# Kernel optimization log

Hardware: AMD Instinct MI355X
Metric: run time of the kernel (lower is better)

## Reference

```python
import jax, jax.numpy as jnp
import numpy as np

N_NODES = 100000
N_EDGES = 3200000
IN_F = 256
OUT_F = 256


def setup_inputs() -> dict:
    key = jax.random.key(0)
    k1, k2, k3, k4, k5, k6 = jax.random.split(key, 6)
    x = jax.random.normal(k1, (N_NODES, IN_F), dtype=jnp.float32)
    edge_row = jnp.sort(jax.random.randint(k2, (N_EDGES,), 0, N_NODES, dtype=jnp.int64))
    edge_col = jax.random.randint(k3, (N_EDGES,), 0, N_NODES, dtype=jnp.int64)
    edge_val = jax.random.uniform(k4, (N_EDGES,), dtype=jnp.float32)
    stdv = 1.0 / np.sqrt(OUT_F)
    weight = jax.random.uniform(k5, (IN_F, OUT_F), dtype=jnp.float32, minval=-stdv, maxval=stdv)
    bias = jax.random.uniform(k6, (OUT_F,), dtype=jnp.float32, minval=-stdv, maxval=stdv)
    return {"x": x, "edge_row": edge_row, "edge_col": edge_col,
            "edge_val": edge_val, "weight": weight, "bias": bias}


def reference(x, edge_row, edge_col, edge_val, weight, bias):
    # support = x @ W  -> [N, out]
    support = jnp.matmul(x, weight)
    # spmm(adj, support): out[r] = sum_e val[e] * support[col[e]] for edges with row[e]==r
    gathered = support[edge_col] * edge_val[:, None]  # [E, out]
    output = jax.ops.segment_sum(gathered, edge_row, num_segments=N_NODES)
    return output + bias
```

## Files before the change

kernel.cpp:

```cpp
#include <hip/hip_runtime.h>
#include <hip/hip_bf16.h>

#define NN 100000
#define NE 3200000
#define NF 256
#define CHUNK 512

typedef __attribute__((ext_vector_type(8))) __bf16 bf16x8;
typedef __attribute__((ext_vector_type(4))) float  f32x4;


__global__ __launch_bounds__(256) void prep_all(const float* __restrict__ w,
                                                __bf16* __restrict__ wfrag,
                                                const float* __restrict__ bias,
                                                float* __restrict__ bias_p,
                                                const int* __restrict__ erow,
                                                int* __restrict__ rowptr) {
    if (blockIdx.x >= 33) {
        const int e = (blockIdx.x - 33) * 256 + threadIdx.x;
        if (e >= NE) return;
        const int r    = erow[e];
        const int prev = (e == 0) ? -1 : erow[e - 1];
        for (int q = prev + 1; q <= r; ++q) rowptr[q] = e;
        if (e == NE - 1) {
            for (int q = r + 1; q <= NN; ++q) rowptr[q] = NE;
        }
        return;
    }
    if (blockIdx.x == 32) {
        const int t = threadIdx.x;
        const int l = t >> 2, b = t & 3;
        bias_p[t] = bias[(l & 3) * 64 + 16 * b + (l >> 2)];
        return;
    }
    const int t = blockIdx.x * 256 + threadIdx.x;
    const int lane = t & 63;
    const int nf   = (t >> 6) & 15;
    const int ks   = t >> 10;
    const int col  = nf * 16 + (lane & 15);
    const int k0   = ks * 32 + (lane >> 4) * 8;
    bf16x8 v;
#pragma unroll
    for (int j = 0; j < 8; ++j) v[j] = (__bf16)w[(k0 + j) * NF + col];
    reinterpret_cast<bf16x8*>(wfrag)[t] = v;
}

__global__ __launch_bounds__(320) void gemm_q(const float* __restrict__ x,
                                              const __bf16* __restrict__ wfrag,
                                              unsigned char* __restrict__ tab,
                                              float* __restrict__ scales) {
    __shared__ __align__(16) __bf16 As[80 * 72];

    const int t    = threadIdx.x;
    const int wv   = t >> 6;
    const int lane = t & 63;
    const int row0 = blockIdx.x * 80;

    f32x4 acc[16];
#pragma unroll
    for (int nf = 0; nf < 16; ++nf) acc[nf] = (f32x4){0.f, 0.f, 0.f, 0.f};

    const int    srow = t >> 2;
    const int    sc   = (t & 3) * 16;
    const float* xp   = x + (size_t)(row0 + srow) * NF + sc;
    char* const  wr   = reinterpret_cast<char*>(As) + srow * 144 + sc * 2;

    const char* const rd =
        reinterpret_cast<const char*>(As) + (wv * 16 + (lane & 15)) * 144 + ((lane >> 4) << 4);

    const bf16x8* wf = reinterpret_cast<const bf16x8*>(wfrag);

    f32x4 s0 = __builtin_nontemporal_load(reinterpret_cast<const f32x4*>(xp));
    f32x4 s1 = __builtin_nontemporal_load(reinterpret_cast<const f32x4*>(xp + 4));
    f32x4 s2 = __builtin_nontemporal_load(reinterpret_cast<const f32x4*>(xp + 8));
    f32x4 s3 = __builtin_nontemporal_load(reinterpret_cast<const f32x4*>(xp + 12));

    for (int p = 0; p < 4; ++p) {
        bf16x8 b0, b1;
        b0[0] = (__bf16)s0.x; b0[1] = (__bf16)s0.y; b0[2] = (__bf16)s0.z; b0[3] = (__bf16)s0.w;
        b0[4] = (__bf16)s1.x; b0[5] = (__bf16)s1.y; b0[6] = (__bf16)s1.z; b0[7] = (__bf16)s1.w;
        b1[0] = (__bf16)s2.x; b1[1] = (__bf16)s2.y; b1[2] = (__bf16)s2.z; b1[3] = (__bf16)s2.w;
        b1[4] = (__bf16)s3.x; b1[5] = (__bf16)s3.y; b1[6] = (__bf16)s3.z; b1[7] = (__bf16)s3.w;
        *reinterpret_cast<bf16x8*>(wr)      = b0;
        *reinterpret_cast<bf16x8*>(wr + 16) = b1;
        __syncthreads();

        if (p < 3) {
            const float* nx = xp + (p + 1) * 64;
            s0 = __builtin_nontemporal_load(reinterpret_cast<const f32x4*>(nx));
            s1 = __builtin_nontemporal_load(reinterpret_cast<const f32x4*>(nx + 4));
            s2 = __builtin_nontemporal_load(reinterpret_cast<const f32x4*>(nx + 8));
            s3 = __builtin_nontemporal_load(reinterpret_cast<const f32x4*>(nx + 12));
        }

        const bf16x8 af0 = *reinterpret_cast<const bf16x8*>(rd);
        const bf16x8 af1 = *reinterpret_cast<const bf16x8*>(rd + 64);
#pragma unroll
        for (int nf = 0; nf < 16; ++nf) {
            const bf16x8 w0 = wf[((p * 2 + 0) * 16 + nf) * 64 + lane];
            acc[nf] = __builtin_amdgcn_mfma_f32_16x16x32_bf16(af0, w0, acc[nf], 0, 0, 0);
        }
#pragma unroll
        for (int nf = 0; nf < 16; ++nf) {
            const bf16x8 w1 = wf[((p * 2 + 1) * 16 + nf) * 64 + lane];
            acc[nf] = __builtin_amdgcn_mfma_f32_16x16x32_bf16(af1, w1, acc[nf], 0, 0, 0);
        }
        __syncthreads();
    }

    const int hi   = lane >> 4;
    const int ccol = lane & 15;

    float m[4];
#pragma unroll
    for (int r = 0; r < 4; ++r) {
        float mm = 0.f;
#pragma unroll
        for (int nf = 0; nf < 16; ++nf) mm = fmaxf(mm, fabsf(acc[nf][r]));
        m[r] = mm;
    }
#pragma unroll
    for (int w = 1; w < 16; w <<= 1) {
#pragma unroll
        for (int r = 0; r < 4; ++r) m[r] = fmaxf(m[r], __shfl_xor(m[r], w, 64));
    }

#pragma unroll
    for (int r = 0; r < 4; ++r) {
        const int   node = row0 + wv * 16 + hi * 4 + r;
        const float isc  = 127.0f / fmaxf(m[r], 1e-30f);
        uint4 pk = {0u, 0u, 0u, 0u};
        unsigned int* pw = reinterpret_cast<unsigned int*>(&pk);
#pragma unroll
        for (int nf = 0; nf < 16; ++nf) {
            const int q = (int)rintf(acc[nf][r] * isc) + 128;
            pw[nf >> 2] |= ((unsigned int)(q & 0xff)) << ((nf & 3) * 8);
        }
        *reinterpret_cast<uint4*>(tab + (size_t)node * 256 + ccol * 16) = pk;
        if (ccol == 0) scales[node] = m[r] * (1.0f / 127.0f);
    }
}

__global__ __launch_bounds__(256) void spmm_f(const unsigned int* __restrict__ tab32,
                                              const int* __restrict__ rowptr,
                                              const int* __restrict__ ecol,
                                              const float* __restrict__ eval,
                                              const float* __restrict__ scales,
                                              const float* __restrict__ bias_p,
                                              float* __restrict__ out) {
    __shared__ int2 buf[CHUNK];

    const int wave = threadIdx.x >> 6;
    const int lane = threadIdx.x & 63;
    const int row  = blockIdx.x * 4 + wave;

    const int bs   = rowptr[blockIdx.x * 4];
    const int bend = rowptr[blockIdx.x * 4 + 4];
    const int rs   = rowptr[row];
    const int re   = rowptr[row + 1];

    float a0 = 0.f, a1 = 0.f, a2 = 0.f, a3 = 0.f, S = 0.f;

    for (int cs = bs; cs < bend; cs += CHUNK) {
        const int cnt = min(CHUNK, bend - cs);
        if (cs != bs) __syncthreads();
        for (int j = threadIdx.x; j < cnt; j += 256) {
            const int   c = ecol[cs + j];
            const float v = eval[cs + j];
            buf[j] = make_int2(c, __float_as_int(v * scales[c]));
        }
        __syncthreads();

        const int lo = max(rs, cs);
        const int hi = min(re, cs + cnt);
#pragma unroll 4
        for (int i = lo; i < hi; ++i) {
            const int2  p = buf[i - cs];
            const float v = __int_as_float(p.y);
            const unsigned int g = tab32[((unsigned)p.x << 6) + lane];
            a0 = fmaf(v, (float)(g & 0xffu), a0);
            a1 = fmaf(v, (float)((g >> 8) & 0xffu), a1);
            a2 = fmaf(v, (float)((g >> 16) & 0xffu), a2);
            a3 = fmaf(v, (float)(g >> 24), a3);
            S += v;
        }
    }

    const f32x4 bp = *reinterpret_cast<const f32x4*>(bias_p + lane * 4);
    const float c128 = 128.0f * S;
    float* op = out + (size_t)row * NF + (lane & 3) * 64 + (lane >> 2);
    __builtin_nontemporal_store(a0 - c128 + bp.x, op);
    __builtin_nontemporal_store(a1 - c128 + bp.y, op + 16);
    __builtin_nontemporal_store(a2 - c128 + bp.z, op + 32);
    __builtin_nontemporal_store(a3 - c128 + bp.w, op + 48);
}

extern "C" void kernel_launch(void* const* d_in, const int* in_sizes, int n_in,
                              void* d_out, int out_size, void* d_ws, size_t ws_size,
                              hipStream_t stream) {
    const float* x    = (const float*)d_in[0];
    const int*   erow = (const int*)d_in[1];
    const int*   ecol = (const int*)d_in[2];
    const float* eval = (const float*)d_in[3];
    const float* w    = (const float*)d_in[4];
    const float* bias = (const float*)d_in[5];
    float*       out  = (float*)d_out;

    unsigned char* tab    = (unsigned char*)d_ws;
    int*           rowptr = (int*)((char*)d_ws + 25600000);
    __bf16*        wfrag  = (__bf16*)((char*)d_ws + 26000016);
    float*         scales = (float*)((char*)d_ws + 26131088);
    float*         bias_p = (float*)((char*)d_ws + 26531088);

    prep_all<<<33 + (NE + 255) / 256, 256, 0, stream>>>(w, wfrag, bias, bias_p,
                                                        erow, rowptr);
    gemm_q<<<NN / 80, 320, 0, stream>>>(x, wfrag, tab, scales);
    spmm_f<<<NN / 4, 256, 0, stream>>>(
        reinterpret_cast<const unsigned int*>(tab), rowptr, ecol, eval, scales,
        bias_p, out);
}
```

Measured before the change: 196.5 us.

## Reuse weight fragments across two row tiles per wave and vectorize rowptr build

The GEMM kernel now uses 128-row blocks of 4 waves, each wave computing two 16-row tiles. Every weight fragment loaded from global memory therefore feeds two MFMAs, halving weight traffic per output row, with bounds clamping for the partial last block. The rowptr construction now has each thread handle 8 sorted edges using vectorized loads, cutting thread count and redundant neighbor reads. Doubling the accumulators raises register pressure, which the launch bounds of 2 blocks per SM try to contain.

Result: slower. 214.2 us (+9.0%).

```diff
diff --git a/kernel.cpp b/kernel.cpp
--- a/kernel.cpp
+++ b/kernel.cpp
@@ -8,6 +8,7 @@
 
 typedef __attribute__((ext_vector_type(8))) __bf16 bf16x8;
 typedef __attribute__((ext_vector_type(4))) float  f32x4;
+typedef __attribute__((ext_vector_type(4))) int    i32x4;
 
 
 __global__ __launch_bounds__(256) void prep_all(const float* __restrict__ w,
@@ -17,13 +18,21 @@
                                                 const int* __restrict__ erow,
                                                 int* __restrict__ rowptr) {
     if (blockIdx.x >= 33) {
-        const int e = (blockIdx.x - 33) * 256 + threadIdx.x;
-        if (e >= NE) return;
-        const int r    = erow[e];
-        const int prev = (e == 0) ? -1 : erow[e - 1];
-        for (int q = prev + 1; q <= r; ++q) rowptr[q] = e;
-        if (e == NE - 1) {
-            for (int q = r + 1; q <= NN; ++q) rowptr[q] = NE;
+        const int t8 = (blockIdx.x - 33) * 256 + threadIdx.x;
+        if (t8 >= NE / 8) return;
+        const int base = t8 * 8;
+        const i32x4 c0 = *reinterpret_cast<const i32x4*>(erow + base);
+        const i32x4 c1 = *reinterpret_cast<const i32x4*>(erow + base + 4);
+        int E[8] = {c0.x, c0.y, c0.z, c0.w, c1.x, c1.y, c1.z, c1.w};
+        int prev = (base == 0) ? -1 : erow[base - 1];
+#pragma unroll
+        for (int j = 0; j < 8; ++j) {
+            const int r = E[j];
+            for (int q = prev + 1; q <= r; ++q) rowptr[q] = base + j;
+            prev = r;
+        }
+        if (base + 8 == NE) {
+            for (int q = prev + 1; q <= NN; ++q) rowptr[q] = NE;
         }
         return;
     }
@@ -45,65 +54,67 @@
     reinterpret_cast<bf16x8*>(wfrag)[t] = v;
 }
 
-__global__ __launch_bounds__(320) void gemm_q(const float* __restrict__ x,
-                                              const __bf16* __restrict__ wfrag,
-                                              unsigned char* __restrict__ tab,
-                                              float* __restrict__ scales) {
-    __shared__ __align__(16) __bf16 As[80 * 72];
+__global__ __launch_bounds__(256, 2) void gemm_q(const float* __restrict__ x,
+                                                 const __bf16* __restrict__ wfrag,
+                                                 unsigned char* __restrict__ tab,
+                                                 float* __restrict__ scales) {
+    __shared__ __align__(16) __bf16 As[128 * 72];
 
     const int t    = threadIdx.x;
     const int wv   = t >> 6;
     const int lane = t & 63;
-    const int row0 = blockIdx.x * 80;
-
-    f32x4 acc[16];
-#pragma unroll
-    for (int nf = 0; nf < 16; ++nf) acc[nf] = (f32x4){0.f, 0.f, 0.f, 0.f};
-
-    const int    srow = t >> 2;
-    const int    sc   = (t & 3) * 16;
-    const float* xp   = x + (size_t)(row0 + srow) * NF + sc;
-    char* const  wr   = reinterpret_cast<char*>(As) + srow * 144 + sc * 2;
+    const int row0 = blockIdx.x * 128;
+
+    f32x4 acc[2][16];
+#pragma unroll
+    for (int rt = 0; rt < 2; ++rt)
+#pragma unroll
+        for (int nf = 0; nf < 16; ++nf) acc[rt][nf] = (f32x4){0.f, 0.f, 0.f, 0.f};
+
+    const int    srow  = t >> 1;
+    const int    row_g = min(row0 + srow, NN - 1);
+    const float* xp    = x + (size_t)row_g * NF + (t & 1) * 32;
+    char* const  wr    = reinterpret_cast<char*>(As) + srow * 144 + (t & 1) * 64;
 
     const char* const rd =
-        reinterpret_cast<const char*>(As) + (wv * 16 + (lane & 15)) * 144 + ((lane >> 4) << 4);
+        reinterpret_cast<const char*>(As) + (wv * 32 + (lane & 15)) * 144 + ((lane >> 4) << 4);
 
     const bf16x8* wf = reinterpret_cast<const bf16x8*>(wfrag);
 
-    f32x4 s0 = __builtin_nontemporal_load(reinterpret_cast<const f32x4*>(xp));
-    f32x4 s1 = __builtin_nontemporal_load(reinterpret_cast<const f32x4*>(xp + 4));
-    f32x4 s2 = __builtin_nontemporal_load(reinterpret_cast<const f32x4*>(xp + 8));
-    f32x4 s3 = __builtin_nontemporal_load(reinterpret_cast<const f32x4*>(xp + 12));
+    f32x4 s[8];
+#pragma unroll
+    for (int i = 0; i < 8; ++i)
+        s[i] = __builtin_nontemporal_load(reinterpret_cast<const f32x4*>(xp + i * 4));
 
     for (int p = 0; p < 4; ++p) {
-        bf16x8 b0, b1;
-        b0[0] = (__bf16)s0.x; b0[1] = (__bf16)s0.y; b0[2] = (__bf16)s0.z; b0[3] = (__bf16)s0.w;
-        b0[4] = (__bf16)s1.x; b0[5] = (__bf16)s1.y; b0[6] = (__bf16)s1.z; b0[7] = (__bf16)s1.w;
-        b1[0] = (__bf16)s2.x; b1[1] = (__bf16)s2.y; b1[2] = (__bf16)s2.z; b1[3] = (__bf16)s2.w;
-        b1[4] = (__bf16)s3.x; b1[5] = (__bf16)s3.y; b1[6] = (__bf16)s3.z; b1[7] = (__bf16)s3.w;
-        *reinterpret_cast<bf16x8*>(wr)      = b0;
-        *reinterpret_cast<bf16x8*>(wr + 16) = b1;
+#pragma unroll
+        for (int i = 0; i < 4; ++i) {
+            bf16x8 b;
+            b[0] = (__bf16)s[2*i].x;   b[1] = (__bf16)s[2*i].y;
+            b[2] = (__bf16)s[2*i].z;   b[3] = (__bf16)s[2*i].w;
+            b[4] = (__bf16)s[2*i+1].x; b[5] = (__bf16)s[2*i+1].y;
+            b[6] = (__bf16)s[2*i+1].z; b[7] = (__bf16)s[2*i+1].w;
+            *reinterpret_cast<bf16x8*>(wr + i * 16) = b;
+        }
         __syncthreads();
 
         if (p < 3) {
-            const float* nx = xp + (p + 1) * 64;
-            s0 = __builtin_nontemporal_load(reinterpret_cast<const f32x4*>(nx));
-            s1 = __builtin_nontemporal_load(reinterpret_cast<const f32x4*>(nx + 4));
-            s2 = __builtin_nontemporal_load(reinterpret_cast<const f32x4*>(nx + 8));
-            s3 = __builtin_nontemporal_load(reinterpret_cast<const f32x4*>(nx + 12));
-        }
-
-        const bf16x8 af0 = *reinterpret_cast<const bf16x8*>(rd);
-        const bf16x8 af1 = *reinterpret_cast<const bf16x8*>(rd + 64);
-#pragma unroll
-        for (int nf = 0; nf < 16; ++nf) {
-            const bf16x8 w0 = wf[((p * 2 + 0) * 16 + nf) * 64 + lane];
-            acc[nf] = __builtin_amdgcn_mfma_f32_16x16x32_bf16(af0, w0, acc[nf], 0, 0, 0);
-        }
-#pragma unroll
-        for (int nf = 0; nf < 16; ++nf) {
-            const bf16x8 w1 = wf[((p * 2 + 1) * 16 + nf) * 64 + lane];
-            acc[nf] = __builtin_amdgcn_mfma_f32_16x16x32_bf16(af1, w1, acc[nf], 0, 0, 0);
+#pragma unroll
+            for (int i = 0; i < 8; ++i)
+                s[i] = __builtin_nontemporal_load(
+                    reinterpret_cast<const f32x4*>(xp + (p + 1) * 64 + i * 4));
+        }
+
+#pragma unroll
+        for (int ksub = 0; ksub < 2; ++ksub) {
+            const bf16x8 af0 = *reinterpret_cast<const bf16x8*>(rd + ksub * 64);
+            const bf16x8 af1 = *reinterpret_cast<const bf16x8*>(rd + 2304 + ksub * 64);
+#pragma unroll
+            for (int nf = 0; nf < 16; ++nf) {
+                const bf16x8 wv8 = wf[((p * 2 + ksub) * 16 + nf) * 64 + lane];
+                acc[0][nf] = __builtin_amdgcn_mfma_f32_16x16x32_bf16(af0, wv8, acc[0][nf], 0, 0, 0);
+                acc[1][nf] = __builtin_amdgcn_mfma_f32_16x16x32_bf16(af1, wv8, acc[1][nf], 0, 0, 0);
+            }
         }
         __syncthreads();
     }
@@ -111,33 +122,38 @@
     const int hi   = lane >> 4;
     const int ccol = lane & 15;
 
-    float m[4];
-#pragma unroll
-    for (int r = 0; r < 4; ++r) {
-        float mm = 0.f;
-#pragma unroll
-        for (int nf = 0; nf < 16; ++nf) mm = fmaxf(mm, fabsf(acc[nf][r]));
-        m[r] = mm;
-    }
-#pragma unroll
-    for (int w = 1; w < 16; w <<= 1) {
-#pragma unroll
-        for (int r = 0; r < 4; ++r) m[r] = fmaxf(m[r], __shfl_xor(m[r], w, 64));
-    }
-
-#pragma unroll
-    for (int r = 0; r < 4; ++r) {
-        const int   node = row0 + wv * 16 + hi * 4 + r;
-        const float isc  = 127.0f / fmaxf(m[r], 1e-30f);
-        uint4 pk = {0u, 0u, 0u, 0u};
-        unsigned int* pw = reinterpret_cast<unsigned int*>(&pk);
-#pragma unroll
-        for (int nf = 0; nf < 16; ++nf) {
-            const int q = (int)rintf(acc[nf][r] * isc) + 128;
-            pw[nf >> 2] |= ((unsigned int)(q & 0xff)) << ((nf & 3) * 8);
-        }
-        *reinterpret_cast<uint4*>(tab + (size_t)node * 256 + ccol * 16) = pk;
-        if (ccol == 0) scales[node] = m[r] * (1.0f / 127.0f);
+#pragma unroll
+    for (int rt = 0; rt < 2; ++rt) {
+        float m[4];
+#pragma unroll
+        for (int r = 0; r < 4; ++r) {
+            float mm = 0.f;
+#pragma unroll
+            for (int nf = 0; nf < 16; ++nf) mm = fmaxf(mm, fabsf(acc[rt][nf][r]));
+            m[r] = mm;
+        }
+#pragma unroll
+        for (int w = 1; w < 16; w <<= 1) {
+#pragma unroll
+            for (int r = 0; r < 4; ++r) m[r] = fmaxf(m[r], __shfl_xor(m[r], w, 64));
+        }
+
+#pragma unroll
+        for (int r = 0; r < 4; ++r) {
+            const int node = row0 + wv * 32 + rt * 16 + hi * 4 + r;
+            if (node < NN) {
+                const float isc = 127.0f / fmaxf(m[r], 1e-30f);
+                uint4 pk = {0u, 0u, 0u, 0u};
+                unsigned int* pw = reinterpret_cast<unsigned int*>(&pk);
+#pragma unroll
+                for (int nf = 0; nf < 16; ++nf) {
+                    const int q = (int)rintf(acc[rt][nf][r] * isc) + 128;
+                    pw[nf >> 2] |= ((unsigned int)(q & 0xff)) << ((nf & 3) * 8);
+                }
+                *reinterpret_cast<uint4*>(tab + (size_t)node * 256 + ccol * 16) = pk;
+                if (ccol == 0) scales[node] = m[r] * (1.0f / 127.0f);
+            }
+        }
     }
 }
 
@@ -212,9 +228,9 @@
     float*         scales = (float*)((char*)d_ws + 26131088);
     float*         bias_p = (float*)((char*)d_ws + 26531088);
 
-    prep_all<<<33 + (NE + 255) / 256, 256, 0, stream>>>(w, wfrag, bias, bias_p,
-                                                        erow, rowptr);
-    gemm_q<<<NN / 80, 320, 0, stream>>>(x, wfrag, tab, scales);
+    prep_all<<<33 + (NE / 8 + 255) / 256, 256, 0, stream>>>(w, wfrag, bias, bias_p,
+                                                            erow, rowptr);
+    gemm_q<<<(NN + 127) / 128, 256, 0, stream>>>(x, wfrag, tab, scales);
     spmm_f<<<NN / 4, 256, 0, stream>>>(
         reinterpret_cast<const unsigned int*>(tab), rowptr, ecol, eval, scales,
         bias_p, out);
```

## Process two rows per wavefront in SpMM with 8-byte gathers per lane

Applied to the files above, without the earlier changes.

The SpMM kernel now gives each half-wave (32 lanes) its own output row, so a block of 256 threads covers 8 rows instead of 4. Each lane gathers 8 bytes (8 int8 features) per edge instead of 4, which halves the number of gather instructions per row. The two half-waves loop to the larger of their two edge counts, and the shorter one feeds zero weights for the extra iterations. The output store order is remapped to match the new lane layout and reads bias directly. The costs are divergence from unequal row lengths within a wave and output stores that are less coalesced.

After: 202.8 us. +3.2%, slower.

```diff
diff --git a/kernel.cpp b/kernel.cpp
--- a/kernel.cpp
+++ b/kernel.cpp
@@ -8,6 +8,7 @@
 
 typedef __attribute__((ext_vector_type(8))) __bf16 bf16x8;
 typedef __attribute__((ext_vector_type(4))) float  f32x4;
+typedef __attribute__((ext_vector_type(2))) unsigned int u32x2;
 
 
 __global__ __launch_bounds__(256) void prep_all(const float* __restrict__ w,
@@ -141,25 +142,27 @@
     }
 }
 
-__global__ __launch_bounds__(256) void spmm_f(const unsigned int* __restrict__ tab32,
+__global__ __launch_bounds__(256) void spmm_h(const unsigned char* __restrict__ tab,
                                               const int* __restrict__ rowptr,
                                               const int* __restrict__ ecol,
                                               const float* __restrict__ eval,
                                               const float* __restrict__ scales,
-                                              const float* __restrict__ bias_p,
+                                              const float* __restrict__ bias,
                                               float* __restrict__ out) {
     __shared__ int2 buf[CHUNK];
 
     const int wave = threadIdx.x >> 6;
     const int lane = threadIdx.x & 63;
-    const int row  = blockIdx.x * 4 + wave;
-
-    const int bs   = rowptr[blockIdx.x * 4];
-    const int bend = rowptr[blockIdx.x * 4 + 4];
+    const int l5   = lane & 31;
+    const int row  = blockIdx.x * 8 + wave * 2 + (lane >> 5);
+
+    const int bs   = rowptr[blockIdx.x * 8];
+    const int bend = rowptr[blockIdx.x * 8 + 8];
     const int rs   = rowptr[row];
     const int re   = rowptr[row + 1];
 
-    float a0 = 0.f, a1 = 0.f, a2 = 0.f, a3 = 0.f, S = 0.f;
+    float a[8] = {0.f, 0.f, 0.f, 0.f, 0.f, 0.f, 0.f, 0.f};
+    float S = 0.f;
 
     for (int cs = bs; cs < bend; cs += CHUNK) {
         const int cnt = min(CHUNK, bend - cs);
@@ -173,26 +176,37 @@
 
         const int lo = max(rs, cs);
         const int hi = min(re, cs + cnt);
-#pragma unroll 4
-        for (int i = lo; i < hi; ++i) {
-            const int2  p = buf[i - cs];
-            const float v = __int_as_float(p.y);
-            const unsigned int g = tab32[((unsigned)p.x << 6) + lane];
-            a0 = fmaf(v, (float)(g & 0xffu), a0);
-            a1 = fmaf(v, (float)((g >> 8) & 0xffu), a1);
-            a2 = fmaf(v, (float)((g >> 16) & 0xffu), a2);
-            a3 = fmaf(v, (float)(g >> 24), a3);
+        int m = hi - lo; m = m < 0 ? 0 : m;
+        const int mo   = __shfl_xor(m, 32, 64);
+        const int mmax = m > mo ? m : mo;
+
+        for (int j = 0; j < mmax; ++j) {
+            const bool act  = j < m;
+            const int  bidx = act ? (lo + j - cs) : 0;
+            const int2 p = buf[bidx];
+            const float v = act ? __int_as_float(p.y) : 0.f;
+            const u32x2 g = *reinterpret_cast<const u32x2*>(
+                tab + ((size_t)(unsigned)p.x << 8) + l5 * 8);
+            a[0] = fmaf(v, (float)(g.x & 0xffu), a[0]);
+            a[1] = fmaf(v, (float)((g.x >> 8) & 0xffu), a[1]);
+            a[2] = fmaf(v, (float)((g.x >> 16) & 0xffu), a[2]);
+            a[3] = fmaf(v, (float)(g.x >> 24), a[3]);
+            a[4] = fmaf(v, (float)(g.y & 0xffu), a[4]);
+            a[5] = fmaf(v, (float)((g.y >> 8) & 0xffu), a[5]);
+            a[6] = fmaf(v, (float)((g.y >> 16) & 0xffu), a[6]);
+            a[7] = fmaf(v, (float)(g.y >> 24), a[7]);
             S += v;
         }
     }
 
-    const f32x4 bp = *reinterpret_cast<const f32x4*>(bias_p + lane * 4);
     const float c128 = 128.0f * S;
-    float* op = out + (size_t)row * NF + (lane & 3) * 64 + (lane >> 2);
-    __builtin_nontemporal_store(a0 - c128 + bp.x, op);
-    __builtin_nontemporal_store(a1 - c128 + bp.y, op + 16);
-    __builtin_nontemporal_store(a2 - c128 + bp.z, op + 32);
-    __builtin_nontemporal_store(a3 - c128 + bp.w, op + 48);
+    float* orow = out + (size_t)row * NF;
+#pragma unroll
+    for (int q = 0; q < 8; ++q) {
+        const int p    = l5 * 8 + q;
+        const int feat = (p & 15) * 16 + (p >> 4);
+        __builtin_nontemporal_store(a[q] - c128 + bias[feat], orow + feat);
+    }
 }
 
 extern "C" void kernel_launch(void* const* d_in, const int* in_sizes, int n_in,
@@ -215,7 +229,5 @@
     prep_all<<<33 + (NE + 255) / 256, 256, 0, stream>>>(w, wfrag, bias, bias_p,
                                                         erow, rowptr);
     gemm_q<<<NN / 80, 320, 0, stream>>>(x, wfrag, tab, scales);
-    spmm_f<<<NN / 4, 256, 0, stream>>>(
-        reinterpret_cast<const unsigned int*>(tab), rowptr, ecol, eval, scales,
-        bias_p, out);
-}
+    spmm_h<<<NN / 8, 256, 0, stream>>>(tab, rowptr, ecol, eval, scales, bias, out);
+}
```
